# Kernel optimization log

Hardware: AMD Instinct MI355X
Metric: run time of the kernel (lower is better)

The kernel has to match this reference:

```python
import jax, jax.numpy as jnp
import numpy as np
import math

D_MODEL = 1024
N_HEADS = 16
D_FF = 4096
D_K = D_MODEL // N_HEADS
B, S = 2, 2048
EPS = 1e-5


def _linear_params(key, fan_in, fan_out):
    kw, kb = jax.random.split(key)
    bound = 1.0 / math.sqrt(fan_in)
    W = jax.random.uniform(kw, (fan_out, fan_in), jnp.float32, -bound, bound)
    b = jax.random.uniform(kb, (fan_out,), jnp.float32, -bound, bound)
    return W, b


def setup_inputs() -> dict:
    key = jax.random.key(0)
    ks = jax.random.split(key, 8)
    x = jax.random.normal(ks[0], (B, S, D_MODEL), jnp.float32)
    # causal mask, broadcast over batch and heads; 0 -> masked
    mask = jnp.tril(jnp.ones((S, S), jnp.int32))[None, None, :, :]
    wq, bq = _linear_params(ks[1], D_MODEL, D_MODEL)
    wk, bk = _linear_params(ks[2], D_MODEL, D_MODEL)
    wv, bv = _linear_params(ks[3], D_MODEL, D_MODEL)
    wo, bo = _linear_params(ks[4], D_MODEL, D_MODEL)
    w1, b1 = _linear_params(ks[5], D_MODEL, D_FF)
    w2, b2 = _linear_params(ks[6], D_FF, D_MODEL)
    g1 = jnp.ones((D_MODEL,), jnp.float32)
    be1 = jnp.zeros((D_MODEL,), jnp.float32)
    g2 = jnp.ones((D_MODEL,), jnp.float32)
    be2 = jnp.zeros((D_MODEL,), jnp.float32)
    return dict(x=x, mask=mask, wq=wq, bq=bq, wk=wk, bk=bk, wv=wv, bv=bv,
                wo=wo, bo=bo, w1=w1, b1=b1, w2=w2, b2=b2,
                g1=g1, be1=be1, g2=g2, be2=be2)


def _layernorm(x, g, b):
    mu = jnp.mean(x, axis=-1, keepdims=True)
    var = jnp.mean(jnp.square(x - mu), axis=-1, keepdims=True)
    return (x - mu) * jax.lax.rsqrt(var + EPS) * g + b


def reference(x, mask, wq, bq, wk, bk, wv, bv, wo, bo, w1, b1, w2, b2, g1, be1, g2, be2):
    Bsz, Sl, _ = x.shape
    def heads(t):  # [B,S,D] -> [B,H,S,d_k]
        return t.reshape(Bsz, Sl, N_HEADS, D_K).transpose(0, 2, 1, 3)
    Q = heads(x @ wq.T + bq)
    K = heads(x @ wk.T + bk)
    V = heads(x @ wv.T + bv)
    scores = jnp.einsum('bhqd,bhkd->bhqk', Q, K) / math.sqrt(D_K)
    scores = jnp.where(mask == 0, jnp.float32(-1e9), scores)
    attn = jax.nn.softmax(scores, axis=-1)
    out = jnp.einsum('bhqk,bhkd->bhqd', attn, V)
    out = out.transpose(0, 2, 1, 3).reshape(Bsz, Sl, D_MODEL)
    attn_out = out @ wo.T + bo
    h = _layernorm(x + attn_out, g1, be1)  # dropout is identity in eval
    ff = jax.nn.relu(h @ w1.T + b1) @ w2.T + b2
    return _layernorm(h + ff, g2, be2)
```

## Files before the change

### kernel.cpp

```cpp
#include <hip/hip_runtime.h>
#include <hip/hip_bf16.h>


using f32x4 = __attribute__((ext_vector_type(4))) float;
using s16x8 = __attribute__((ext_vector_type(8))) short;

constexpr int D_MODEL = 1024;
constexpr int D_FF    = 4096;
constexpr int DK      = 64;
constexpr int BB      = 2;
constexpr int SS      = 2048;
constexpr int NTOK    = BB * SS;

#define QSCALE 0.18033688011112042f

__device__ __forceinline__ ushort f2bf(float f) {
    unsigned u = __float_as_uint(f);
    u += 0x7fffu + ((u >> 16) & 1u);
    return (ushort)(u >> 16);
}

__device__ __forceinline__ float bflo(uint v) { return __uint_as_float(v << 16); }
__device__ __forceinline__ float bfhi(uint v) { return __uint_as_float(v & 0xffff0000u); }

__device__ __forceinline__ float ex2(float x) {
    float r;
    asm("v_exp_f32 %0, %1" : "=v"(r) : "v"(x));
    return r;
}

__device__ __forceinline__ void gload_lds16(const void* g, void* l) {
    __builtin_amdgcn_global_load_lds(
        (const __attribute__((address_space(1))) void*)g,
        (__attribute__((address_space(3))) void*)l, 16, 0, 0);
}

struct CvtArgs { const float* src[7]; ushort* dst[7]; };

__global__ __launch_bounds__(256) void cvt_all(CvtArgs a) {
    constexpr long S[8] = {0L<<20, 1L<<20, 2L<<20, 3L<<20,
                           4L<<20, 8L<<20, 12L<<20, 16L<<20};
    long i = ((long)blockIdx.x * 256 + threadIdx.x) * 4;
    int s = 0;
#pragma unroll
    for (int j = 1; j < 7; ++j) if (i >= S[j]) s = j;
    long off = i - S[s];
    float4 v = *(const float4*)(a.src[s] + off);
    ushort4 o;
    o.x = f2bf(v.x); o.y = f2bf(v.y); o.z = f2bf(v.z); o.w = f2bf(v.w);
    *(ushort4*)(a.dst[s] + off) = o;
}

template <bool RELU, bool OUTBF16>
__global__ __launch_bounds__(256, 2) void gemm_bt(
        const ushort* __restrict__ A, const ushort* __restrict__ W,
        const float* __restrict__ bias,
        void* __restrict__ Cout, int M, int N, int Klen, int ldk, int gx, int splitk) {
    __shared__ __align__(16) char Asb[2][128 * 128];
    __shared__ __align__(16) char Bsb[2][128 * 128];

    const int nwg = (int)gridDim.x;
    const int id  = (int)blockIdx.x;
    const int sw  = (id & 7) * (nwg >> 3) + (id >> 3);
    const int tps = nwg / splitk;
    const int s   = sw / tps;
    const int rem = sw - s * tps;
    const int bx  = rem % gx, by = rem / gx;

    const int t  = threadIdx.x;
    const int l  = t & 63;
    const int w  = t >> 6;
    const int wr = w >> 1, wc = w & 1;
    const int li = l & 15, g = l >> 4;
    const int bm0 = by << 7;
    const int bn0 = bx << 7;
    const int kbase = s * Klen;

    f32x4 acc[4][4];
#pragma unroll
    for (int m = 0; m < 4; ++m)
#pragma unroll
        for (int n = 0; n < 4; ++n)
            acc[m][n] = (f32x4){0.f, 0.f, 0.f, 0.f};

    const int rsub = l >> 3, slot = l & 7;
    const int swzel = (((slot * 16) ^ (rsub << 4)) >> 1);

    auto stage = [&](int buf, int k0) {
#pragma unroll
        for (int i = 0; i < 4; ++i) {
            const int rbase = i * 32 + w * 8;
            gload_lds16(A + (size_t)(bm0 + rbase + rsub) * ldk + kbase + k0 + swzel,
                        Asb[buf] + rbase * 128);
            gload_lds16(W + (size_t)(bn0 + rbase + rsub) * ldk + kbase + k0 + swzel,
                        Bsb[buf] + rbase * 128);
        }
    };

    const int nk = Klen >> 6;
    stage(0, 0);
    __syncthreads();

    for (int tt = 0; tt < nk; ++tt) {
        const int cur = tt & 1;
        if (tt + 1 < nk) stage(cur ^ 1, (tt + 1) << 6);
#pragma unroll
        for (int ks = 0; ks < 2; ++ks) {
            s16x8 af[4], bfr[4];
#pragma unroll
            for (int m = 0; m < 4; ++m) {
                int row = wr * 64 + m * 16 + li;
                af[m] = *(const s16x8*)(Asb[cur] + row * 128 + (((ks * 4 + g) * 16) ^ ((row & 7) << 4)));
            }
#pragma unroll
            for (int n = 0; n < 4; ++n) {
                int row = wc * 64 + n * 16 + li;
                bfr[n] = *(const s16x8*)(Bsb[cur] + row * 128 + (((ks * 4 + g) * 16) ^ ((row & 7) << 4)));
            }
            __builtin_amdgcn_s_setprio(1);
#pragma unroll
            for (int m = 0; m < 4; ++m)
#pragma unroll
                for (int n = 0; n < 4; ++n)
                    acc[m][n] = __builtin_amdgcn_mfma_f32_16x16x32_bf16(af[m], bfr[n], acc[m][n], 0, 0, 0);
            __builtin_amdgcn_s_setprio(0);
        }
        __syncthreads();
    }

    const bool dobias = (s == 0);
    float* Cf = (float*)Cout + (size_t)s * M * N;
#pragma unroll
    for (int m = 0; m < 4; ++m) {
        int row0 = bm0 + wr * 64 + m * 16 + g * 4;
#pragma unroll
        for (int n = 0; n < 4; ++n) {
            int col = bn0 + wc * 64 + n * 16 + li;
            float bsv = dobias ? bias[col] : 0.f;
#pragma unroll
            for (int r = 0; r < 4; ++r) {
                float v = acc[m][n][r] + bsv;
                if (RELU) v = fmaxf(v, 0.f);
                size_t idx = (size_t)(row0 + r) * N + col;
                if (OUTBF16) ((ushort*)Cout)[idx] = f2bf(v);
                else         Cf[idx] = v;
            }
        }
    }
}

__global__ __launch_bounds__(256, 2) void gemm_qkvt(
        const ushort* __restrict__ xb, const ushort* __restrict__ wqkb,
        const ushort* __restrict__ wvb,
        const float* __restrict__ bq, const float* __restrict__ bk,
        const float* __restrict__ bv,
        ushort* __restrict__ QKb, ushort* __restrict__ VtG) {
    __shared__ __align__(16) char Asb[2][128 * 128];
    __shared__ __align__(16) char Bsb[2][128 * 128];

    const int id = (int)blockIdx.x;
    const int sw = (id & 7) * 96 + (id >> 3);
    const bool vt = (sw >= 512);
    int bx, by, N;
    const ushort *A, *W;
    if (!vt) { bx = sw % 16;          by = sw / 16;          A = xb;  W = wqkb; N = 2048; }
    else     { int s2 = sw - 512; bx = s2 % 32; by = s2 / 32; A = wvb; W = xb;  N = 4096; }

    const int t  = threadIdx.x;
    const int l  = t & 63;
    const int w  = t >> 6;
    const int wr = w >> 1, wc = w & 1;
    const int li = l & 15, g = l >> 4;
    const int bm0 = by << 7;
    const int bn0 = bx << 7;

    f32x4 acc[4][4];
#pragma unroll
    for (int m = 0; m < 4; ++m)
#pragma unroll
        for (int n = 0; n < 4; ++n)
            acc[m][n] = (f32x4){0.f, 0.f, 0.f, 0.f};

    const int rsub = l >> 3, slot = l & 7;
    const int swzel = (((slot * 16) ^ (rsub << 4)) >> 1);

    auto stage = [&](int buf, int k0) {
#pragma unroll
        for (int i = 0; i < 4; ++i) {
            const int rbase = i * 32 + w * 8;
            gload_lds16(A + (size_t)(bm0 + rbase + rsub) * 1024 + k0 + swzel,
                        Asb[buf] + rbase * 128);
            gload_lds16(W + (size_t)(bn0 + rbase + rsub) * 1024 + k0 + swzel,
                        Bsb[buf] + rbase * 128);
        }
    };

    stage(0, 0);
    __syncthreads();

    for (int tt = 0; tt < 16; ++tt) {
        const int cur = tt & 1;
        if (tt + 1 < 16) stage(cur ^ 1, (tt + 1) << 6);
#pragma unroll
        for (int ks = 0; ks < 2; ++ks) {
            s16x8 af[4], bfr[4];
#pragma unroll
            for (int m = 0; m < 4; ++m) {
                int row = wr * 64 + m * 16 + li;
                af[m] = *(const s16x8*)(Asb[cur] + row * 128 + (((ks * 4 + g) * 16) ^ ((row & 7) << 4)));
            }
#pragma unroll
            for (int n = 0; n < 4; ++n) {
                int row = wc * 64 + n * 16 + li;
                bfr[n] = *(const s16x8*)(Bsb[cur] + row * 128 + (((ks * 4 + g) * 16) ^ ((row & 7) << 4)));
            }
            __builtin_amdgcn_s_setprio(1);
#pragma unroll
            for (int m = 0; m < 4; ++m)
#pragma unroll
                for (int n = 0; n < 4; ++n)
                    acc[m][n] = __builtin_amdgcn_mfma_f32_16x16x32_bf16(af[m], bfr[n], acc[m][n], 0, 0, 0);
            __builtin_amdgcn_s_setprio(0);
        }
        __syncthreads();
    }

#pragma unroll
    for (int m = 0; m < 4; ++m) {
        int row0 = bm0 + wr * 64 + m * 16 + g * 4;
#pragma unroll
        for (int n = 0; n < 4; ++n) {
            int col = bn0 + wc * 64 + n * 16 + li;
            if (!vt) {
                float bsv = (col < 1024) ? bq[col] : bk[col - 1024];
                float sc  = (col < 1024) ? QSCALE : 1.f;
#pragma unroll
                for (int r = 0; r < 4; ++r) {
                    float v = (acc[m][n][r] + bsv) * sc;
                    QKb[(size_t)(row0 + r) * 2048 + col] = f2bf(v);
                }
            } else {
#pragma unroll
                for (int r = 0; r < 4; ++r) {
                    float v = acc[m][n][r] + bv[row0 + r];
                    VtG[(size_t)(row0 + r) * 4096 + col] = f2bf(v);
                }
            }
        }
    }
}

__global__ __launch_bounds__(256, 4) void attn_kernel(
        const ushort* __restrict__ QKb, const ushort* __restrict__ VtG,
        ushort* __restrict__ po, float* __restrict__ ml) {
    __shared__ __align__(16) char Ks[2][64 * 128];
    __shared__ __align__(16) char Vs[2][64 * 128];
    __shared__ __align__(16) char Ps[4][16 * 128];

    const int t  = threadIdx.x;
    const int l  = t & 63;
    const int w  = t >> 6;
    const int li = l & 15, g = l >> 4;
    const int bx = (int)blockIdx.x;
    const int h  = blockIdx.y;
    const int z  = (int)blockIdx.z;
    const int b    = z & 1;
    const int half = z >> 1;

    const ushort* Kp = QKb + (size_t)(b * SS) * 2048 + 1024 + h * DK;
    const ushort* Vp = VtG + (size_t)(h * DK) * NTOK + b * SS;

    const int rsub = l >> 3, slot = l & 7;
    const int swzsrc = (slot * 16) ^ (rsub << 4);

    auto stage = [&](int buf, int kt) {
#pragma unroll
        for (int c = 0; c < 2; ++c) {
            int row0 = (w + c * 4) * 8;
            gload_lds16((const char*)(Kp + (size_t)(kt + row0 + rsub) * 2048) + swzsrc,
                        Ks[buf] + row0 * 128);
            gload_lds16((const char*)(Vp + (size_t)(row0 + rsub) * NTOK + kt) + swzsrc,
                        Vs[buf] + row0 * 128);
        }
    };

    char* Pw = Ps[w];
    const int rswz = (li & 7) << 4;

    for (int ss = 0; ss < 2; ++ss) {
        const int stripe = ss ? bx : (SS / 64 - 1 - bx);
        const int qb = stripe * 64;
        const int qw = qb + w * 16;

        const ushort* Qp = QKb + (size_t)(b * SS + qw) * 2048 + h * DK;
        s16x8 qf[2];
#pragma unroll
        for (int ds = 0; ds < 2; ++ds)
            qf[ds] = *(const s16x8*)(Qp + li * 2048 + ds * 32 + g * 8);

        f32x4 o[4];
#pragma unroll
        for (int d = 0; d < 4; ++d) o[d] = (f32x4){0.f, 0.f, 0.f, 0.f};
        float m_ = -1e30f, ls = 0.f;

        const int ntt  = stripe + 1;
        const int tbeg = half ? (ntt >> 1) : 0;
        const int tend = half ? ntt : (ntt >> 1);
        const int ntH  = tend - tbeg;

        if (ntH > 0) {
            stage(0, tbeg * 64);
            __syncthreads();

            for (int tt = 0; tt < ntH; ++tt) {
                const int kt = (tbeg + tt) * 64;
                const int cur = tt & 1;
                if (tt + 1 < ntH) stage(cur ^ 1, kt + 64);

                f32x4 sa[4];
#pragma unroll
                for (int ks = 0; ks < 4; ++ks) sa[ks] = (f32x4){0.f, 0.f, 0.f, 0.f};
#pragma unroll
                for (int ks = 0; ks < 4; ++ks) {
                    int row = ks * 16 + li;
#pragma unroll
                    for (int ds = 0; ds < 2; ++ds) {
                        s16x8 kf = *(const s16x8*)(Ks[cur] + row * 128 + ((ds * 64 + g * 16) ^ rswz));
                        __builtin_amdgcn_s_setprio(1);
                        sa[ks] = __builtin_amdgcn_mfma_f32_16x16x32_bf16(kf, qf[ds], sa[ks], 0, 0, 0);
                        __builtin_amdgcn_s_setprio(0);
                    }
                }

                const bool maskt = (tbeg + tt == ntt - 1);
                float p[4][4];
                float pmax = -1e30f;
#pragma unroll
                for (int ks = 0; ks < 4; ++ks)
#pragma unroll
                    for (int r = 0; r < 4; ++r) {
                        float sv = sa[ks][r];
                        if (maskt && (kt + ks * 16 + g * 4 + r > qw + li)) sv = -1e30f;
                        p[ks][r] = sv;
                        pmax = fmaxf(pmax, sv);
                    }

                if (!__all(pmax <= m_ + 11.5f)) {
                    float mx = fmaxf(pmax, __shfl_xor(pmax, 16));
                    mx = fmaxf(mx, __shfl_xor(mx, 32));
                    float nm = fmaxf(m_, mx);
                    float fs = ex2(m_ - nm);
                    m_ = nm;
                    ls *= fs;
                    float fsr[4];
#pragma unroll
                    for (int r = 0; r < 4; ++r) fsr[r] = __shfl(fs, g * 4 + r);
#pragma unroll
                    for (int d = 0; d < 4; ++d)
#pragma unroll
                        for (int r = 0; r < 4; ++r) o[d][r] *= fsr[r];
                }
                float rs = 0.f;
#pragma unroll
                for (int ks = 0; ks < 4; ++ks)
#pragma unroll
                    for (int r = 0; r < 4; ++r) {
                        p[ks][r] = ex2(p[ks][r] - m_);
                        rs += p[ks][r];
                    }
                rs += __shfl_xor(rs, 16);
                rs += __shfl_xor(rs, 32);
                ls += rs;

#pragma unroll
                for (int ks = 0; ks < 4; ++ks) {
                    uint u0, u1;
                    asm("v_cvt_pk_bf16_f32 %0, %1, %2" : "=v"(u0) : "v"(p[ks][0]), "v"(p[ks][1]));
                    asm("v_cvt_pk_bf16_f32 %0, %1, %2" : "=v"(u1) : "v"(p[ks][2]), "v"(p[ks][3]));
                    uint2 uv; uv.x = u0; uv.y = u1;
                    *(uint2*)(Pw + li * 128 + ((ks * 32 + g * 8) ^ rswz)) = uv;
                }

                s16x8 pf[2];
#pragma unroll
                for (int ks2 = 0; ks2 < 2; ++ks2)
                    pf[ks2] = *(const s16x8*)(Pw + li * 128 + ((ks2 * 64 + g * 16) ^ rswz));
#pragma unroll
                for (int dblk = 0; dblk < 4; ++dblk) {
                    int vrow = dblk * 16 + li;
#pragma unroll
                    for (int ks2 = 0; ks2 < 2; ++ks2) {
                        s16x8 vf = *(const s16x8*)(Vs[cur] + vrow * 128 + ((ks2 * 64 + g * 16) ^ rswz));
                        __builtin_amdgcn_s_setprio(1);
                        o[dblk] = __builtin_amdgcn_mfma_f32_16x16x32_bf16(pf[ks2], vf, o[dblk], 0, 0, 0);
                        __builtin_amdgcn_s_setprio(0);
                    }
                }
                __syncthreads();
            }
        }

#pragma unroll
        for (int r = 0; r < 4; ++r) {
            ushort* pp = po + ((((size_t)(half * 2 + b)) * SS + qw + g * 4 + r) * 16 + h) * 64;
#pragma unroll
            for (int dblk = 0; dblk < 4; ++dblk)
                pp[dblk * 16 + li] = f2bf(o[dblk][r]);
        }
        if (l < 16) {
            size_t mrow = (((size_t)(half * 2 + b)) * SS + qw + l) * 16 + h;
            ml[mrow * 2]     = m_;
            ml[mrow * 2 + 1] = ls;
        }
    }
}

__global__ __launch_bounds__(256) void attn_combine(
        const ushort* __restrict__ po, const float* __restrict__ ml,
        ushort* __restrict__ ctx) {
    const int idx = blockIdx.x * 256 + threadIdx.x;
    const int row = idx >> 4;
    const int d4  = (idx & 15) * 4;
    const int HR  = 2 * SS * 16;

    float m0 = ml[(size_t)row * 2],        l0 = ml[(size_t)row * 2 + 1];
    float m1 = ml[(size_t)(HR + row) * 2], l1 = ml[(size_t)(HR + row) * 2 + 1];
    float mx = fmaxf(m0, m1);
    float w0 = ex2(m0 - mx), w1 = ex2(m1 - mx);
    float inv = 1.0f / (l0 * w0 + l1 * w1);

    uint2 a = *(const uint2*)(po + (size_t)row * 64 + d4);
    uint2 c = *(const uint2*)(po + (size_t)(HR + row) * 64 + d4);
    float v0 = (bflo(a.x) * w0 + bflo(c.x) * w1) * inv;
    float v1 = (bfhi(a.x) * w0 + bfhi(c.x) * w1) * inv;
    float v2 = (bflo(a.y) * w0 + bflo(c.y) * w1) * inv;
    float v3 = (bfhi(a.y) * w0 + bfhi(c.y) * w1) * inv;
    ushort4 o;
    o.x = f2bf(v0); o.y = f2bf(v1); o.z = f2bf(v2); o.w = f2bf(v3);
    *(ushort4*)(ctx + (size_t)(row >> 4) * 1024 + (row & 15) * 64 + d4) = o;
}

template <bool WBF, bool X3>
__global__ __launch_bounds__(256) void ln_fused(
        const float* __restrict__ xa, const float* __restrict__ xb,
        const float* __restrict__ xc,
        const float* __restrict__ gamma, const float* __restrict__ beta,
        float* __restrict__ outf, ushort* __restrict__ outb) {
    const int row = blockIdx.x;
    const int t   = threadIdx.x;
    const size_t off = (size_t)row * D_MODEL + t * 4;
    float4 a = *(const float4*)(xa + off);
    float4 c = *(const float4*)(xb + off);
    float z0 = a.x + c.x, z1 = a.y + c.y, z2 = a.z + c.z, z3 = a.w + c.w;
    if constexpr (X3) {
        float4 d = *(const float4*)(xc + off);
        z0 += d.x; z1 += d.y; z2 += d.z; z3 += d.w;
    }
    float sum = z0 + z1 + z2 + z3;
    float sq  = z0 * z0 + z1 * z1 + z2 * z2 + z3 * z3;
#pragma unroll
    for (int o = 1; o < 64; o <<= 1) {
        sum += __shfl_xor(sum, o);
        sq  += __shfl_xor(sq, o);
    }
    __shared__ float s1[4], s2[4];
    if ((t & 63) == 0) { s1[t >> 6] = sum; s2[t >> 6] = sq; }
    __syncthreads();
    float tot = s1[0] + s1[1] + s1[2] + s1[3];
    float tsq = s2[0] + s2[1] + s2[2] + s2[3];
    const float invn = 1.0f / (float)D_MODEL;
    float mu  = tot * invn;
    float var = tsq * invn - mu * mu;
    float rstd = rsqrtf(var + 1e-5f);
    float4 gv = *(const float4*)(gamma + t * 4);
    float4 bv = *(const float4*)(beta + t * 4);
    float y0 = (z0 - mu) * rstd * gv.x + bv.x;
    float y1 = (z1 - mu) * rstd * gv.y + bv.y;
    float y2 = (z2 - mu) * rstd * gv.z + bv.z;
    float y3 = (z3 - mu) * rstd * gv.w + bv.w;
    float4 y = {y0, y1, y2, y3};
    *(float4*)(outf + off) = y;
    if constexpr (WBF) {
        ushort4 u;
        u.x = f2bf(y0); u.y = f2bf(y1); u.z = f2bf(y2); u.w = f2bf(y3);
        *(ushort4*)(outb + off) = u;
    }
}

extern "C" void kernel_launch(void* const* d_in, const int* in_sizes, int n_in,
                              void* d_out, int out_size, void* d_ws, size_t ws_size,
                              hipStream_t stream) {
    const float* x   = (const float*)d_in[0];
    const float* wq  = (const float*)d_in[2];  const float* bq  = (const float*)d_in[3];
    const float* wk  = (const float*)d_in[4];  const float* bk  = (const float*)d_in[5];
    const float* wv  = (const float*)d_in[6];  const float* bv  = (const float*)d_in[7];
    const float* wo  = (const float*)d_in[8];  const float* bo  = (const float*)d_in[9];
    const float* w1  = (const float*)d_in[10]; const float* b1  = (const float*)d_in[11];
    const float* w2  = (const float*)d_in[12]; const float* b2  = (const float*)d_in[13];
    const float* g1  = (const float*)d_in[14]; const float* be1 = (const float*)d_in[15];
    const float* g2  = (const float*)d_in[16]; const float* be2 = (const float*)d_in[17];
    float* out = (float*)d_out;

    char* ws = (char*)d_ws;
    const size_t MB = 1u << 20;
    ushort* wqkb = (ushort*)(ws + 0 * MB);
    ushort* wvb  = (ushort*)(ws + 4 * MB);
    ushort* wob  = (ushort*)(ws + 6 * MB);
    ushort* w1b  = (ushort*)(ws + 8 * MB);
    ushort* w2b  = (ushort*)(ws + 16 * MB);
    ushort* xb   = (ushort*)(ws + 24 * MB);
    ushort* QKb  = (ushort*)(ws + 32 * MB);
    ushort* VtG  = (ushort*)(ws + 48 * MB);
    ushort* ctx  = (ushort*)(ws + 56 * MB);
    ushort* po   = (ushort*)(ws + 64 * MB);
    float*  ml   = (float*)(ws + 81 * MB);
    float*  p0   = (float*)(ws + 64 * MB);
    float*  p1   = (float*)(ws + 80 * MB);
    float*  h    = (float*)(ws + 96 * MB);
    ushort* hb   = (ushort*)(ws + 112 * MB);
    ushort* ffib = (ushort*)(ws + 24 * MB);

    CvtArgs ca;
    ca.src[0] = wq; ca.dst[0] = wqkb;
    ca.src[1] = wk; ca.dst[1] = wqkb + D_MODEL * D_MODEL;
    ca.src[2] = wv; ca.dst[2] = wvb;
    ca.src[3] = wo; ca.dst[3] = wob;
    ca.src[4] = w1; ca.dst[4] = w1b;
    ca.src[5] = w2; ca.dst[5] = w2b;
    ca.src[6] = x;  ca.dst[6] = xb;
    cvt_all<<<dim3(16384), dim3(256), 0, stream>>>(ca);

    dim3 blk(256);
    gemm_qkvt<<<dim3(768), blk, 0, stream>>>(xb, wqkb, wvb, bq, bk, bv, QKb, VtG);

    attn_kernel<<<dim3(SS / 128, 16, 2 * BB), blk, 0, stream>>>(QKb, VtG, po, ml);
    attn_combine<<<dim3(4096), blk, 0, stream>>>(po, ml, ctx);

    gemm_bt<false, false><<<dim3(512), blk, 0, stream>>>(
        ctx, wob, bo, p0, NTOK, D_MODEL, 512, D_MODEL, 8, 2);
    ln_fused<true, true><<<dim3(NTOK), blk, 0, stream>>>(x, p0, p1, g1, be1, h, hb);

    gemm_bt<true, true><<<dim3(1024), blk, 0, stream>>>(
        hb, w1b, b1, ffib, NTOK, D_FF, D_MODEL, D_MODEL, 32, 1);
    gemm_bt<false, false><<<dim3(512), blk, 0, stream>>>(
        ffib, w2b, b2, p0, NTOK, D_MODEL, 2048, D_FF, 8, 2);
    ln_fused<false, true><<<dim3(NTOK), blk, 0, stream>>>(h, p0, p1, g2, be2, out, nullptr);
}
```

Baseline: 245.5 us.

## Add 256x256-tile 8-wave pipelined GEMM for the FFN up-projection with ReLU

Replaces the generic 128x128 gemm_bt for the first FFN matmul with a dedicated kernel that uses 256x256 output tiles, 512 threads and double-buffered LDS. Loads go directly to LDS with explicit vmcnt/lgkmcnt waits and barriers, so the next K-slice is staged while MFMAs run on the current one. The aim is more operand reuse per tile and less load latency exposed on the largest GEMM. In exchange it needs about 128KB of LDS per block and only launches one wave of 256 blocks, and its epilogue writes scalar bf16 values.

```diff
diff --git a/kernel.cpp b/kernel.cpp
--- a/kernel.cpp
+++ b/kernel.cpp
@@ -35,6 +35,19 @@
         (__attribute__((address_space(3))) void*)l, 16, 0, 0);
 }
 
+__device__ __forceinline__ void wait_vm4() {
+    asm volatile("s_waitcnt vmcnt(4)" ::: "memory");
+    __builtin_amdgcn_sched_barrier(0);
+}
+__device__ __forceinline__ void wait_vm0() {
+    asm volatile("s_waitcnt vmcnt(0)" ::: "memory");
+    __builtin_amdgcn_sched_barrier(0);
+}
+__device__ __forceinline__ void wait_lgkm0() {
+    asm volatile("s_waitcnt lgkmcnt(0)" ::: "memory");
+    __builtin_amdgcn_sched_barrier(0);
+}
+
 struct CvtArgs { const float* src[7]; ushort* dst[7]; };
 
 __global__ __launch_bounds__(256) void cvt_all(CvtArgs a) {
@@ -49,6 +62,140 @@
     ushort4 o;
     o.x = f2bf(v.x); o.y = f2bf(v.y); o.z = f2bf(v.z); o.w = f2bf(v.w);
     *(ushort4*)(a.dst[s] + off) = o;
+}
+
+__global__ __launch_bounds__(512, 2) void gemm256_relu(
+        const ushort* __restrict__ A, const ushort* __restrict__ Wt,
+        const float* __restrict__ bias, ushort* __restrict__ C,
+        int M, int N, int K) {
+    __shared__ __align__(16) char Als[2][2][128 * 128];
+    __shared__ __align__(16) char Bls[2][2][128 * 128];
+
+    const int nwg = (int)gridDim.x;
+    const int id  = (int)blockIdx.x;
+    const int sw  = (id & 7) * (nwg >> 3) + (id >> 3);
+    const int gx  = N >> 8;
+    const int bx  = sw % gx, by = sw / gx;
+    const int bm0 = by << 8, bn0 = bx << 8;
+
+    const int t  = threadIdx.x;
+    const int l  = t & 63;
+    const int w  = t >> 6;
+    const int li = l & 15, g = l >> 4;
+    const int wm = w >> 2, wn = w & 3;
+
+    const int srow  = w * 8 + (l >> 3);
+    const int scolb = (l & 7) * 16;
+    const int svz   = (scolb ^ ((srow & 4) << 3)) >> 1;
+    const int nk    = K >> 6;
+
+    auto stA = [&](int buf, int half, int kt) {
+        if (kt >= nk) return;
+        const ushort* src = A + (size_t)(bm0 + half * 128 + srow) * K + kt * 64 + svz;
+        char* dst = Als[buf][half] + w * 1024;
+        gload_lds16(src, dst);
+        gload_lds16(src + (size_t)64 * K, dst + 8192);
+    };
+    auto stB = [&](int buf, int half, int kt) {
+        if (kt >= nk) return;
+        const ushort* src = Wt + (size_t)(bn0 + half * 128 + srow) * K + kt * 64 + svz;
+        char* dst = Bls[buf][half] + w * 1024;
+        gload_lds16(src, dst);
+        gload_lds16(src + (size_t)64 * K, dst + 8192);
+    };
+
+    const int rdsw = (li & 4) << 3;
+
+    f32x4 acc[8][4];
+#pragma unroll
+    for (int m = 0; m < 8; ++m)
+#pragma unroll
+        for (int n = 0; n < 4; ++n)
+            acc[m][n] = (f32x4){0.f, 0.f, 0.f, 0.f};
+
+    auto ldA2 = [&](int buf, int q, s16x8 af[2][2]) {
+#pragma unroll
+        for (int m2 = 0; m2 < 2; ++m2)
+#pragma unroll
+            for (int kk = 0; kk < 2; ++kk)
+                af[m2][kk] = *(const s16x8*)(Als[buf][wm] +
+                    ((q * 2 + m2) * 16 + li) * 128 + ((kk * 64 + g * 16) ^ rdsw));
+    };
+    auto ldB8 = [&](int buf, s16x8 bfr[4][2]) {
+#pragma unroll
+        for (int nf = 0; nf < 4; ++nf)
+#pragma unroll
+            for (int kk = 0; kk < 2; ++kk)
+                bfr[nf][kk] = *(const s16x8*)(Bls[buf][wn >> 1] +
+                    ((wn & 1) * 64 + nf * 16 + li) * 128 + ((kk * 64 + g * 16) ^ rdsw));
+    };
+    auto mfmaq = [&](int q, s16x8 af[2][2], s16x8 bfr[4][2], int wm_mode) {
+        __builtin_amdgcn_s_barrier();
+        wait_lgkm0();
+        __builtin_amdgcn_s_setprio(1);
+#pragma unroll
+        for (int m2 = 0; m2 < 2; ++m2)
+#pragma unroll
+            for (int nf = 0; nf < 4; ++nf)
+#pragma unroll
+            for (int kk = 0; kk < 2; ++kk)
+                acc[q * 2 + m2][nf] = __builtin_amdgcn_mfma_f32_16x16x32_bf16(
+                    af[m2][kk], bfr[nf][kk], acc[q * 2 + m2][nf], 0, 0, 0);
+        __builtin_amdgcn_s_setprio(0);
+        if (wm_mode == 4) wait_vm4();
+        else if (wm_mode == 0) wait_vm0();
+        __builtin_amdgcn_s_barrier();
+    };
+
+    stB(0, 0, 0); stB(0, 1, 0);
+    stA(0, 0, 0); stA(0, 1, 0);
+    stB(1, 0, 1); stB(1, 1, 1);
+    wait_vm4();
+    __builtin_amdgcn_s_barrier();
+
+    const int ni = nk >> 1;
+    for (int i = 0; i < ni; ++i) {
+        const int t0 = 2 * i;
+        const bool last = (i == ni - 1);
+        {
+            s16x8 bfr[4][2];
+            { ldB8(0, bfr); s16x8 af[2][2]; ldA2(0, 0, af);
+              stA(1, 0, t0 + 1);                      mfmaq(0, af, bfr, -1); }
+            { s16x8 af[2][2]; ldA2(0, 1, af);
+              stA(1, 1, t0 + 1); stB(0, 0, t0 + 2);   mfmaq(1, af, bfr, -1); }
+            { s16x8 af[2][2]; ldA2(0, 2, af);
+              stB(0, 1, t0 + 2);                      mfmaq(2, af, bfr, -1); }
+            { s16x8 af[2][2]; ldA2(0, 3, af);
+                                                      mfmaq(3, af, bfr, last ? 0 : 4); }
+        }
+        {
+            s16x8 bfr[4][2];
+            { ldB8(1, bfr); s16x8 af[2][2]; ldA2(1, 0, af);
+              stA(0, 0, t0 + 2);                      mfmaq(0, af, bfr, -1); }
+            { s16x8 af[2][2]; ldA2(1, 1, af);
+              stA(0, 1, t0 + 2);                      mfmaq(1, af, bfr, -1); }
+            { s16x8 af[2][2]; ldA2(1, 2, af);
+              stB(1, 0, t0 + 3);                      mfmaq(2, af, bfr, -1); }
+            { s16x8 af[2][2]; ldA2(1, 3, af);
+              stB(1, 1, t0 + 3);
+                                                      mfmaq(3, af, bfr, last ? -1 : 4); }
+        }
+    }
+
+#pragma unroll
+    for (int mf = 0; mf < 8; ++mf) {
+        int row0 = bm0 + wm * 128 + mf * 16 + g * 4;
+#pragma unroll
+        for (int nf = 0; nf < 4; ++nf) {
+            int col = bn0 + wn * 64 + nf * 16 + li;
+            float bsv = bias[col];
+#pragma unroll
+            for (int r = 0; r < 4; ++r) {
+                float v = fmaxf(acc[mf][nf][r] + bsv, 0.f);
+                C[(size_t)(row0 + r) * N + col] = f2bf(v);
+            }
+        }
+    }
 }
 
 template <bool RELU, bool OUTBF16>
@@ -540,8 +687,8 @@
         ctx, wob, bo, p0, NTOK, D_MODEL, 512, D_MODEL, 8, 2);
     ln_fused<true, true><<<dim3(NTOK), blk, 0, stream>>>(x, p0, p1, g1, be1, h, hb);
 
-    gemm_bt<true, true><<<dim3(1024), blk, 0, stream>>>(
-        hb, w1b, b1, ffib, NTOK, D_FF, D_MODEL, D_MODEL, 32, 1);
+    gemm256_relu<<<dim3(256), dim3(512), 0, stream>>>(hb, w1b, b1, ffib, NTOK, D_FF, D_MODEL);
+
     gemm_bt<false, false><<<dim3(512), blk, 0, stream>>>(
         ffib, w2b, b2, p0, NTOK, D_MODEL, 2048, D_FF, 8, 2);
     ln_fused<false, true><<<dim3(NTOK), blk, 0, stream>>>(h, p0, p1, g2, be2, out, nullptr);
```

Result: faster. 236.1 us (-3.8%).
